# Kernel tuning notes

Measured on AMD Instinct MI355X. Metric: run time of the kernel, lower is better.

The kernel has to match this reference:

```python
import jax, jax.numpy as jnp
import numpy as np


def _conv1x1(x, W, b):
    # 1x1 conv == per-pixel channel matmul: x [B,C,H,W], W [O,C], b [O]
    return jnp.einsum('bchw,oc->bohw', x, W) + b[None, :, None, None]


def setup_inputs() -> dict:
    key = jax.random.key(0)
    ks = jax.random.split(key, 9)
    B, C, H, W = 16, 512, 32, 32
    s = 1.0 / np.sqrt(C)
    inp = {
        'x': jax.random.normal(ks[0], (B, C, H, W), dtype=jnp.float32),
        'Wq': jax.random.normal(ks[1], (C, C), dtype=jnp.float32) * s,
        'bq': jax.random.normal(ks[2], (C,), dtype=jnp.float32) * 0.01,
        'Wk': jax.random.normal(ks[3], (C, C), dtype=jnp.float32) * s,
        'bk': jax.random.normal(ks[4], (C,), dtype=jnp.float32) * 0.01,
        'Wv': jax.random.normal(ks[5], (C, C), dtype=jnp.float32) * s,
        'bv': jax.random.normal(ks[6], (C,), dtype=jnp.float32) * 0.01,
        'Wo': jax.random.normal(ks[7], (C, C), dtype=jnp.float32) * s,
        'bo': jax.random.normal(ks[8], (C,), dtype=jnp.float32) * 0.01,
    }
    return inp


def reference(x, Wq, bq, Wk, bk, Wv, bv, Wo, bo):
    B, C, H, W = x.shape
    q = _conv1x1(x, Wq, bq)
    k = _conv1x1(x, Wk, bk)
    v = _conv1x1(x, Wv, bv)
    hw = H * W
    qf = q.reshape(B, C, hw)  # [B,C,HW]
    kf = k.reshape(B, C, hw)
    vf = v.reshape(B, C, hw)
    # scores[b,i,j] = sum_c q[b,c,i] * k[b,c,j], scaled by c^-0.5
    scores = jnp.einsum('bci,bcj->bij', qf, kf) * (C ** -0.5)
    attn = jax.nn.softmax(scores, axis=2)  # softmax over keys j
    # out[b,c,i] = sum_j v[b,c,j] * attn[b,i,j]
    out = jnp.einsum('bcj,bij->bci', vf, attn).reshape(B, C, H, W)
    out = _conv1x1(out, Wo, bo)
    return x + out
```

## Files before the change

kernel.cpp:

```cpp
#include <hip/hip_runtime.h>
#include <hip/hip_bf16.h>
#include <math.h>


typedef __bf16 bf16x8 __attribute__((ext_vector_type(8)));
typedef float  f32x4  __attribute__((ext_vector_type(4)));

__device__ __forceinline__ unsigned short f2bf(float f) {
    unsigned u = __float_as_uint(f);
    u += 0x7fff + ((u >> 16) & 1);
    return (unsigned short)(u >> 16);
}

__device__ __forceinline__ void gload_lds16(const void* g, void* l) {
    __builtin_amdgcn_global_load_lds(
        (const __attribute__((address_space(1))) void*)g,
        (__attribute__((address_space(3))) void*)l, 16, 0, 0);
}

template<bool OUT_F32, int BIAS_MODE, bool RESID, int EXPM>
__global__ __launch_bounds__(256) void gemm_bt_mfma(
    const unsigned short* __restrict__ A, const unsigned short* __restrict__ B,
    void* __restrict__ Cout, const float* __restrict__ bias,
    const float* __restrict__ resid, float* __restrict__ lsum,
    int M, int N, int K, int ldA, int ldB,
    long sA, long sB, long sC, long sR,
    int ln_nn, int ln_pb, float scale)
{
    __shared__ unsigned short Als[2][128 * 32];
    __shared__ unsigned short Bls[2][128 * 32];

    const int L   = blockIdx.x;
    const int xcd = L & 7;
    const int idx = L >> 3;
    const int bz  = xcd * 2 + (idx >> ln_pb);
    const int w   = idx & ((1 << ln_pb) - 1);
    const int m0  = (w >> ln_nn) << 7;
    const int n0  = (w & ((1 << ln_nn) - 1)) << 7;

    A += bz * sA;
    B += bz * sB;

    const int tid  = threadIdx.x;
    const int lane = tid & 63;
    const int wave = tid >> 6;
    const int wm   = wave >> 1;
    const int wn   = wave & 1;

    const int ar = lane >> 2;
    const int ak = (lane & 3) * 8;

    const unsigned short* agp = A + (long)(m0 + wave * 16 + ar) * ldA + ak;
    const unsigned short* bgp = B + (long)(n0 + wave * 16 + ar) * ldB + ak;
    const long aj = 64L * ldA;
    const long bj = 64L * ldB;
    unsigned short* al0 = Als[0] + wave * 512;
    unsigned short* al0h = Als[0] + (wave + 4) * 512;
    unsigned short* al1 = Als[1] + wave * 512;
    unsigned short* al1h = Als[1] + (wave + 4) * 512;
    unsigned short* bl0 = Bls[0] + wave * 512;
    unsigned short* bl0h = Bls[0] + (wave + 4) * 512;
    unsigned short* bl1 = Bls[1] + wave * 512;
    unsigned short* bl1h = Bls[1] + (wave + 4) * 512;

    const int fr = lane & 15;
    const int fq = lane >> 4;

    f32x4 acc[4][4] = {};

    for (int k0 = 0; k0 < K; k0 += 64) {
        gload_lds16(agp,           al0);
        gload_lds16(agp + aj,      al0h);
        gload_lds16(agp + 32,      al1);
        gload_lds16(agp + 32 + aj, al1h);
        gload_lds16(bgp,           bl0);
        gload_lds16(bgp + bj,      bl0h);
        gload_lds16(bgp + 32,      bl1);
        gload_lds16(bgp + 32 + bj, bl1h);
        agp += 64; bgp += 64;
        __syncthreads();

        #pragma unroll
        for (int p = 0; p < 2; ++p) {
            bf16x8 af[4], bfr[4];
            #pragma unroll
            for (int mt = 0; mt < 4; ++mt)
                af[mt] = *(const bf16x8*)&Als[p][(wm * 64 + mt * 16 + fr) * 32 + fq * 8];
            #pragma unroll
            for (int nt = 0; nt < 4; ++nt)
                bfr[nt] = *(const bf16x8*)&Bls[p][(wn * 64 + nt * 16 + fr) * 32 + fq * 8];

            #pragma unroll
            for (int mt = 0; mt < 4; ++mt)
                #pragma unroll
                for (int nt = 0; nt < 4; ++nt)
                    acc[mt][nt] = __builtin_amdgcn_mfma_f32_16x16x32_bf16(
                        af[mt], bfr[nt], acc[mt][nt], 0, 0, 0);
        }
        __syncthreads();
    }

    float* Cf = (float*)Cout + bz * sC;
    unsigned short* Ch = (unsigned short*)Cout + bz * sC;
    if (RESID) resid += bz * sR;

    if (EXPM == 1) {
        float* lrow = lsum + bz * (long)M;
        #pragma unroll
        for (int mt = 0; mt < 4; ++mt) {
            const int row = m0 + wm * 64 + mt * 16 + fq * 4;
            #pragma unroll
            for (int r = 0; r < 4; ++r) {
                float rs = 0.0f;
                #pragma unroll
                for (int nt = 0; nt < 4; ++nt) {
                    const int col = n0 + wn * 64 + nt * 16 + fr;
                    const float e = __expf(acc[mt][nt][r] * scale);
                    rs += e;
                    Ch[(long)(row + r) * N + col] = f2bf(e);
                }
                rs += __shfl_xor(rs, 1);
                rs += __shfl_xor(rs, 2);
                rs += __shfl_xor(rs, 4);
                rs += __shfl_xor(rs, 8);
                if (fr == 0) atomicAdd(&lrow[row + r], rs);
            }
        }
    } else {
        float linv[4][4];
        if (EXPM == 2) {
            const float* lrow = lsum + bz * (long)M;
            #pragma unroll
            for (int mt = 0; mt < 4; ++mt)
                #pragma unroll
                for (int r = 0; r < 4; ++r)
                    linv[mt][r] = 1.0f / lrow[m0 + wm * 64 + mt * 16 + fq * 4 + r];
        }
        #pragma unroll
        for (int nt = 0; nt < 4; ++nt) {
            const int col = n0 + wn * 64 + nt * 16 + fr;
            const float bn = (BIAS_MODE == 2) ? bias[col] : 0.0f;
            #pragma unroll
            for (int mt = 0; mt < 4; ++mt) {
                const int row = m0 + wm * 64 + mt * 16 + fq * 4;
                #pragma unroll
                for (int r = 0; r < 4; ++r) {
                    float val = acc[mt][nt][r] + bn;
                    if (BIAS_MODE == 1) val += bias[row + r];
                    if (EXPM == 2) val *= linv[mt][r];
                    const long idx = (long)(row + r) * N + col;
                    if (RESID) val += resid[idx];
                    if (OUT_F32) Cf[idx] = val;
                    else         Ch[idx] = f2bf(val);
                }
            }
        }
    }
}

__global__ __launch_bounds__(256) void prep_all(
    const float* __restrict__ x, unsigned short* __restrict__ xT,
    const float* __restrict__ Wq, const float* __restrict__ Wk,
    const float* __restrict__ Wv, const float* __restrict__ Wo,
    const float* __restrict__ bq, const float* __restrict__ bk,
    unsigned short* __restrict__ Wb, float* __restrict__ biasqk,
    float* __restrict__ lsum)
{
    const int b = blockIdx.x;
    const int t = threadIdx.x;
    if (b < 8192) {
        __shared__ float tl[32][33];
        const int batch = b >> 9;
        const int rem = b & 511;
        const int p0 = (rem & 31) * 32;
        const int c0 = (rem >> 5) * 32;
        const float* xb = x + (long)batch * 524288;
        unsigned short* xTb = xT + (long)batch * 524288;
        const int tx = t & 31;
        const int ty = t >> 5;
        #pragma unroll
        for (int i = 0; i < 4; ++i)
            tl[ty + 8 * i][tx] = xb[(long)(c0 + ty + 8 * i) * 1024 + p0 + tx];
        __syncthreads();
        #pragma unroll
        for (int i = 0; i < 4; ++i)
            xTb[(long)(p0 + ty + 8 * i) * 512 + c0 + tx] = f2bf(tl[tx][ty + 8 * i]);
    } else if (b < 9216) {
        const int wb = b - 8192;
        const float* srcs[4] = {Wq, Wk, Wv, Wo};
        const float* s = srcs[wb >> 8];
        unsigned short* d = Wb + (long)(wb >> 8) * 262144;
        const int i = ((wb & 255) * 256 + t) * 4;
        const float4 f = *(const float4*)(s + i);
        ushort4 h;
        h.x = f2bf(f.x); h.y = f2bf(f.y); h.z = f2bf(f.z); h.w = f2bf(f.w);
        *(ushort4*)(d + i) = h;
    } else {
        biasqk[t]       = bq[t];
        biasqk[256 + t] = bq[256 + t];
        biasqk[512 + t] = bk[t];
        biasqk[768 + t] = bk[256 + t];
        #pragma unroll
        for (int i = 0; i < 64; ++i) lsum[i * 256 + t] = 0.0f;
    }
}

extern "C" void kernel_launch(void* const* d_in, const int* in_sizes, int n_in,
                              void* d_out, int out_size, void* d_ws, size_t ws_size,
                              hipStream_t stream)
{
    const float* x  = (const float*)d_in[0];
    const float* Wq = (const float*)d_in[1];
    const float* bq = (const float*)d_in[2];
    const float* Wk = (const float*)d_in[3];
    const float* bk = (const float*)d_in[4];
    const float* Wv = (const float*)d_in[5];
    const float* bv = (const float*)d_in[6];
    const float* Wo = (const float*)d_in[7];
    const float* bo = (const float*)d_in[8];
    float* out = (float*)d_out;

    const int Bn = 16, C = 512, HW = 1024;
    const long CHW = (long)C * HW;
    const long SHW = (long)HW * HW;

    unsigned short* xT   = (unsigned short*)d_ws;
    unsigned short* qkT  = xT + Bn * CHW;
    unsigned short* vB   = qkT + Bn * SHW;
    unsigned short* expS = vB + Bn * CHW;
    unsigned short* Wb   = expS + Bn * SHW;
    float* biasqk = (float*)(Wb + 4 * 262144);
    float* lsum   = biasqk + 1024;
    unsigned short* OT = xT;

    unsigned short* Wvb = Wb + 2 * 262144;
    unsigned short* Wob = Wb + 3 * 262144;

    const dim3 blk(256);
    const float scale = 0.044194173824159216f;

    prep_all<<<dim3(9217), blk, 0, stream>>>(x, xT, Wq, Wk, Wv, Wo, bq, bk,
                                             Wb, biasqk, lsum);

    gemm_bt_mfma<false, 2, false, 0><<<dim3(1024), blk, 0, stream>>>(
        xT, Wb, qkT, biasqk, nullptr, nullptr,
        HW, 2 * C, C, C, C, CHW, 0, SHW, 0, 3, 6, 0.0f);

    gemm_bt_mfma<false, 1, false, 0><<<dim3(512), blk, 0, stream>>>(
        Wvb, xT, vB, bv, nullptr, nullptr,
        C, HW, C, C, C, 0, CHW, CHW, 0, 3, 5, 0.0f);

    gemm_bt_mfma<false, 0, false, 1><<<dim3(1024), blk, 0, stream>>>(
        qkT, qkT + C, expS, nullptr, nullptr, lsum,
        HW, HW, C, 2 * C, 2 * C, SHW, SHW, SHW, 0, 3, 6, scale);

    gemm_bt_mfma<false, 0, false, 2><<<dim3(512), blk, 0, stream>>>(
        expS, vB, OT, nullptr, nullptr, lsum,
        HW, C, HW, HW, HW, SHW, CHW, CHW, 0, 2, 5, 0.0f);

    gemm_bt_mfma<true, 1, true, 0><<<dim3(512), blk, 0, stream>>>(
        Wob, OT, out, bo, x, nullptr,
        C, HW, C, C, C, 0, CHW, CHW, CHW, 3, 5, 0.0f);
}
```

Measured before the change: 219.6 us.

## Switch GEMMs to 32x32x16 MFMA with swizzled LDS and fuse QK/V launches

Each wave now computes its 64x64 tile with 2x2 32x32x16 bf16 MFMAs instead of 4x4 16x16x32. This cuts LDS fragment reads and MFMA instruction count per k-step. The LDS layout gains an XOR swizzle on the k-offset, applied on both the global-to-LDS load and the fragment read, to reduce bank conflicts. The QK and V projection GEMMs are merged into one launch that splits the grid by block index, removing a kernel launch and letting both fill the GPU together. The epilogue index mapping is rewritten for the 32x32 accumulator layout, which risks correctness errors and adds register pressure.

```diff
diff --git a/kernel.cpp b/kernel.cpp
--- a/kernel.cpp
+++ b/kernel.cpp
@@ -4,7 +4,7 @@
 
 
 typedef __bf16 bf16x8 __attribute__((ext_vector_type(8)));
-typedef float  f32x4  __attribute__((ext_vector_type(4)));
+typedef float  f32x16 __attribute__((ext_vector_type(16)));
 
 __device__ __forceinline__ unsigned short f2bf(float f) {
     unsigned u = __float_as_uint(f);
@@ -18,28 +18,33 @@
         (__attribute__((address_space(3))) void*)l, 16, 0, 0);
 }
 
+struct GemmP {
+    const unsigned short* A;
+    const unsigned short* B;
+    void* C;
+    const float* bias;
+    const float* resid;
+    float* lsum;
+    int M, N, K, ldA, ldB;
+    long sA, sB, sC, sR;
+    int ln_nn, ln_pb;
+    float scale;
+};
+
 template<bool OUT_F32, int BIAS_MODE, bool RESID, int EXPM>
-__global__ __launch_bounds__(256) void gemm_bt_mfma(
-    const unsigned short* __restrict__ A, const unsigned short* __restrict__ B,
-    void* __restrict__ Cout, const float* __restrict__ bias,
-    const float* __restrict__ resid, float* __restrict__ lsum,
-    int M, int N, int K, int ldA, int ldB,
-    long sA, long sB, long sC, long sR,
-    int ln_nn, int ln_pb, float scale)
-{
-    __shared__ unsigned short Als[2][128 * 32];
-    __shared__ unsigned short Bls[2][128 * 32];
-
-    const int L   = blockIdx.x;
+__device__ __forceinline__ void gemm_body(const GemmP p, int L,
+                                          unsigned short* Als,
+                                          unsigned short* Bls)
+{
     const int xcd = L & 7;
     const int idx = L >> 3;
-    const int bz  = xcd * 2 + (idx >> ln_pb);
-    const int w   = idx & ((1 << ln_pb) - 1);
-    const int m0  = (w >> ln_nn) << 7;
-    const int n0  = (w & ((1 << ln_nn) - 1)) << 7;
-
-    A += bz * sA;
-    B += bz * sB;
+    const int bz  = xcd * 2 + (idx >> p.ln_pb);
+    const int w   = idx & ((1 << p.ln_pb) - 1);
+    const int m0  = (w >> p.ln_nn) << 7;
+    const int n0  = (w & ((1 << p.ln_nn) - 1)) << 7;
+
+    const unsigned short* A = p.A + bz * p.sA;
+    const unsigned short* B = p.B + bz * p.sB;
 
     const int tid  = threadIdx.x;
     const int lane = tid & 63;
@@ -48,27 +53,29 @@
     const int wn   = wave & 1;
 
     const int ar = lane >> 2;
-    const int ak = (lane & 3) * 8;
-
-    const unsigned short* agp = A + (long)(m0 + wave * 16 + ar) * ldA + ak;
-    const unsigned short* bgp = B + (long)(n0 + wave * 16 + ar) * ldB + ak;
-    const long aj = 64L * ldA;
-    const long bj = 64L * ldB;
-    unsigned short* al0 = Als[0] + wave * 512;
-    unsigned short* al0h = Als[0] + (wave + 4) * 512;
-    unsigned short* al1 = Als[1] + wave * 512;
-    unsigned short* al1h = Als[1] + (wave + 4) * 512;
-    unsigned short* bl0 = Bls[0] + wave * 512;
-    unsigned short* bl0h = Bls[0] + (wave + 4) * 512;
-    unsigned short* bl1 = Bls[1] + wave * 512;
-    unsigned short* bl1h = Bls[1] + (wave + 4) * 512;
-
-    const int fr = lane & 15;
-    const int fq = lane >> 4;
-
-    f32x4 acc[4][4] = {};
-
-    for (int k0 = 0; k0 < K; k0 += 64) {
+    const int ak = ((lane & 3) ^ (ar & 2)) * 8;
+
+    const unsigned short* agp = A + (long)(m0 + wave * 16 + ar) * p.ldA + ak;
+    const unsigned short* bgp = B + (long)(n0 + wave * 16 + ar) * p.ldB + ak;
+    const long aj = 64L * p.ldA;
+    const long bj = 64L * p.ldB;
+
+    unsigned short* al0  = Als + wave * 512;
+    unsigned short* al0h = Als + (wave + 4) * 512;
+    unsigned short* al1  = Als + 4096 + wave * 512;
+    unsigned short* al1h = Als + 4096 + (wave + 4) * 512;
+    unsigned short* bl0  = Bls + wave * 512;
+    unsigned short* bl0h = Bls + (wave + 4) * 512;
+    unsigned short* bl1  = Bls + 4096 + wave * 512;
+    unsigned short* bl1h = Bls + 4096 + (wave + 4) * 512;
+
+    const int ln31 = lane & 31;
+    const int hi   = lane >> 5;
+    const int swz  = (ln31 & 2) << 3;
+
+    f32x16 acc[2][2] = {};
+
+    for (int k0 = 0; k0 < p.K; k0 += 64) {
         gload_lds16(agp,           al0);
         gload_lds16(agp + aj,      al0h);
         gload_lds16(agp + 32,      al1);
@@ -81,81 +88,114 @@
         __syncthreads();
 
         #pragma unroll
-        for (int p = 0; p < 2; ++p) {
-            bf16x8 af[4], bfr[4];
-            #pragma unroll
-            for (int mt = 0; mt < 4; ++mt)
-                af[mt] = *(const bf16x8*)&Als[p][(wm * 64 + mt * 16 + fr) * 32 + fq * 8];
-            #pragma unroll
-            for (int nt = 0; nt < 4; ++nt)
-                bfr[nt] = *(const bf16x8*)&Bls[p][(wn * 64 + nt * 16 + fr) * 32 + fq * 8];
-
-            #pragma unroll
-            for (int mt = 0; mt < 4; ++mt)
-                #pragma unroll
-                for (int nt = 0; nt < 4; ++nt)
-                    acc[mt][nt] = __builtin_amdgcn_mfma_f32_16x16x32_bf16(
-                        af[mt], bfr[nt], acc[mt][nt], 0, 0, 0);
+        for (int pp = 0; pp < 2; ++pp) {
+            const unsigned short* Ap = Als + pp * 4096;
+            const unsigned short* Bp = Bls + pp * 4096;
+            bf16x8 af[2][2], bfr[2][2];
+            #pragma unroll
+            for (int mt = 0; mt < 2; ++mt)
+                #pragma unroll
+                for (int ks = 0; ks < 2; ++ks)
+                    af[mt][ks] = *(const bf16x8*)
+                        &Ap[(wm * 64 + mt * 32 + ln31) * 32 +
+                            ((ks * 16 + hi * 8) ^ swz)];
+            #pragma unroll
+            for (int nt = 0; nt < 2; ++nt)
+                #pragma unroll
+                for (int ks = 0; ks < 2; ++ks)
+                    bfr[nt][ks] = *(const bf16x8*)
+                        &Bp[(wn * 64 + nt * 32 + ln31) * 32 +
+                            ((ks * 16 + hi * 8) ^ swz)];
+
+            #pragma unroll
+            for (int ks = 0; ks < 2; ++ks)
+                #pragma unroll
+                for (int mt = 0; mt < 2; ++mt)
+                    #pragma unroll
+                    for (int nt = 0; nt < 2; ++nt)
+                        acc[mt][nt] = __builtin_amdgcn_mfma_f32_32x32x16_bf16(
+                            af[mt][ks], bfr[nt][ks], acc[mt][nt], 0, 0, 0);
         }
         __syncthreads();
     }
 
-    float* Cf = (float*)Cout + bz * sC;
-    unsigned short* Ch = (unsigned short*)Cout + bz * sC;
-    if (RESID) resid += bz * sR;
+    float* Cf = (float*)p.C + bz * p.sC;
+    unsigned short* Ch = (unsigned short*)p.C + bz * p.sC;
+    const float* resid = RESID ? (p.resid + bz * p.sR) : nullptr;
+    const int N = p.N;
 
     if (EXPM == 1) {
-        float* lrow = lsum + bz * (long)M;
-        #pragma unroll
-        for (int mt = 0; mt < 4; ++mt) {
-            const int row = m0 + wm * 64 + mt * 16 + fq * 4;
-            #pragma unroll
-            for (int r = 0; r < 4; ++r) {
+        float* lrow = p.lsum + bz * (long)p.M;
+        #pragma unroll
+        for (int mt = 0; mt < 2; ++mt) {
+            #pragma unroll
+            for (int r = 0; r < 16; ++r) {
+                const int row = m0 + wm * 64 + mt * 32 +
+                                (r & 3) + 8 * (r >> 2) + 4 * hi;
                 float rs = 0.0f;
                 #pragma unroll
-                for (int nt = 0; nt < 4; ++nt) {
-                    const int col = n0 + wn * 64 + nt * 16 + fr;
-                    const float e = __expf(acc[mt][nt][r] * scale);
+                for (int nt = 0; nt < 2; ++nt) {
+                    const int col = n0 + wn * 64 + nt * 32 + ln31;
+                    const float e = __expf(acc[mt][nt][r] * p.scale);
                     rs += e;
-                    Ch[(long)(row + r) * N + col] = f2bf(e);
+                    Ch[(long)row * N + col] = f2bf(e);
                 }
                 rs += __shfl_xor(rs, 1);
                 rs += __shfl_xor(rs, 2);
                 rs += __shfl_xor(rs, 4);
                 rs += __shfl_xor(rs, 8);
-                if (fr == 0) atomicAdd(&lrow[row + r], rs);
+                rs += __shfl_xor(rs, 16);
+                if (ln31 == 0) atomicAdd(&lrow[row], rs);
             }
         }
     } else {
-        float linv[4][4];
-        if (EXPM == 2) {
-            const float* lrow = lsum + bz * (long)M;
-            #pragma unroll
-            for (int mt = 0; mt < 4; ++mt)
-                #pragma unroll
-                for (int r = 0; r < 4; ++r)
-                    linv[mt][r] = 1.0f / lrow[m0 + wm * 64 + mt * 16 + fq * 4 + r];
-        }
-        #pragma unroll
-        for (int nt = 0; nt < 4; ++nt) {
-            const int col = n0 + wn * 64 + nt * 16 + fr;
-            const float bn = (BIAS_MODE == 2) ? bias[col] : 0.0f;
-            #pragma unroll
-            for (int mt = 0; mt < 4; ++mt) {
-                const int row = m0 + wm * 64 + mt * 16 + fq * 4;
-                #pragma unroll
-                for (int r = 0; r < 4; ++r) {
+        #pragma unroll
+        for (int mt = 0; mt < 2; ++mt) {
+            float linv[16];
+            if (EXPM == 2) {
+                const float* lrow = p.lsum + bz * (long)p.M;
+                #pragma unroll
+                for (int r = 0; r < 16; ++r)
+                    linv[r] = 1.0f / lrow[m0 + wm * 64 + mt * 32 +
+                                          (r & 3) + 8 * (r >> 2) + 4 * hi];
+            }
+            #pragma unroll
+            for (int nt = 0; nt < 2; ++nt) {
+                const int col = n0 + wn * 64 + nt * 32 + ln31;
+                const float bn = (BIAS_MODE == 2) ? p.bias[col] : 0.0f;
+                #pragma unroll
+                for (int r = 0; r < 16; ++r) {
+                    const int row = m0 + wm * 64 + mt * 32 +
+                                    (r & 3) + 8 * (r >> 2) + 4 * hi;
                     float val = acc[mt][nt][r] + bn;
-                    if (BIAS_MODE == 1) val += bias[row + r];
-                    if (EXPM == 2) val *= linv[mt][r];
-                    const long idx = (long)(row + r) * N + col;
-                    if (RESID) val += resid[idx];
-                    if (OUT_F32) Cf[idx] = val;
-                    else         Ch[idx] = f2bf(val);
+                    if (BIAS_MODE == 1) val += p.bias[row];
+                    if (EXPM == 2) val *= linv[r];
+                    const long o = (long)row * N + col;
+                    if (RESID) val += resid[o];
+                    if (OUT_F32) Cf[o] = val;
+                    else         Ch[o] = f2bf(val);
                 }
             }
         }
     }
+}
+
+template<bool OUT_F32, int BIAS_MODE, bool RESID, int EXPM>
+__global__ __launch_bounds__(256) void gemm_bt_mfma(GemmP p)
+{
+    __shared__ unsigned short Als[2 * 4096];
+    __shared__ unsigned short Bls[2 * 4096];
+    gemm_body<OUT_F32, BIAS_MODE, RESID, EXPM>(p, blockIdx.x, Als, Bls);
+}
+
+__global__ __launch_bounds__(256) void gemm_qkv_fused(GemmP pqk, GemmP pv, int split)
+{
+    __shared__ unsigned short Als[2 * 4096];
+    __shared__ unsigned short Bls[2 * 4096];
+    if ((int)blockIdx.x < split)
+        gemm_body<false, 2, false, 0>(pqk, blockIdx.x, Als, Bls);
+    else
+        gemm_body<false, 1, false, 0>(pv, blockIdx.x - split, Als, Bls);
 }
 
 __global__ __launch_bounds__(256) void prep_all(
@@ -242,23 +282,21 @@
     prep_all<<<dim3(9217), blk, 0, stream>>>(x, xT, Wq, Wk, Wv, Wo, bq, bk,
                                              Wb, biasqk, lsum);
 
-    gemm_bt_mfma<false, 2, false, 0><<<dim3(1024), blk, 0, stream>>>(
-        xT, Wb, qkT, biasqk, nullptr, nullptr,
-        HW, 2 * C, C, C, C, CHW, 0, SHW, 0, 3, 6, 0.0f);
-
-    gemm_bt_mfma<false, 1, false, 0><<<dim3(512), blk, 0, stream>>>(
-        Wvb, xT, vB, bv, nullptr, nullptr,
-        C, HW, C, C, C, 0, CHW, CHW, 0, 3, 5, 0.0f);
-
-    gemm_bt_mfma<false, 0, false, 1><<<dim3(1024), blk, 0, stream>>>(
-        qkT, qkT + C, expS, nullptr, nullptr, lsum,
-        HW, HW, C, 2 * C, 2 * C, SHW, SHW, SHW, 0, 3, 6, scale);
-
-    gemm_bt_mfma<false, 0, false, 2><<<dim3(512), blk, 0, stream>>>(
-        expS, vB, OT, nullptr, nullptr, lsum,
-        HW, C, HW, HW, HW, SHW, CHW, CHW, 0, 2, 5, 0.0f);
-
-    gemm_bt_mfma<true, 1, true, 0><<<dim3(512), blk, 0, stream>>>(
-        Wob, OT, out, bo, x, nullptr,
-        C, HW, C, C, C, 0, CHW, CHW, CHW, 3, 5, 0.0f);
-}
+    GemmP pqk = { xT, Wb, qkT, biasqk, nullptr, nullptr,
+                  HW, 2 * C, C, C, C, CHW, 0, SHW, 0, 3, 6, 0.0f };
+    GemmP pv  = { Wvb, xT, vB, bv, nullptr, nullptr,
+                  C, HW, C, C, C, 0, CHW, CHW, 0, 3, 5, 0.0f };
+    gemm_qkv_fused<<<dim3(1536), blk, 0, stream>>>(pqk, pv, 1024);
+
+    GemmP ps  = { qkT, qkT + C, expS, nullptr, nullptr, lsum,
+                  HW, HW, C, 2 * C, 2 * C, SHW, SHW, SHW, 0, 3, 6, scale };
+    gemm_bt_mfma<false, 0, false, 1><<<dim3(1024), blk, 0, stream>>>(ps);
+
+    GemmP po  = { expS, vB, OT, nullptr, nullptr, lsum,
+                  HW, C, HW, HW, HW, SHW, CHW, CHW, 0, 2, 5, 0.0f };
+    gemm_bt_mfma<false, 0, false, 2><<<dim3(512), blk, 0, stream>>>(po);
+
+    GemmP pout = { Wob, OT, out, bo, x, nullptr,
+                   C, HW, C, C, C, 0, CHW, CHW, CHW, 3, 5, 0.0f };
+    gemm_bt_mfma<true, 1, true, 0><<<dim3(512), blk, 0, stream>>>(pout);
+}
```

After: 237.3 us. 1.08x slower.
